# Optimization experiments

Hardware: AMD Instinct MI355X
Metric: run time of the kernel (lower is better)

Reference implementation:

```python
import jax, jax.numpy as jnp
import numpy as np


def setup_inputs() -> dict:
    key = jax.random.key(0)
    ks = jax.random.split(key, 13)
    B, W, C = 16, 2048, 512
    inp = {
        "X_sfr": jax.random.normal(ks[0], (B, W, C), dtype=jnp.float32),
        "adj_matrix": jax.random.normal(ks[1], (B, C, C), dtype=jnp.float32),
        "log_temp": jnp.zeros((1,), dtype=jnp.float32),
        "wq": jax.random.normal(ks[2], (1,), dtype=jnp.float32),
        "bq": jax.random.normal(ks[3], (1,), dtype=jnp.float32),
        "wk": jax.random.normal(ks[4], (1,), dtype=jnp.float32),
        "bk": jax.random.normal(ks[5], (1,), dtype=jnp.float32),
        "wv": jax.random.normal(ks[6], (1,), dtype=jnp.float32),
        "bv": jax.random.normal(ks[7], (1,), dtype=jnp.float32),
        "wmu": jax.random.normal(ks[8], (1,), dtype=jnp.float32),
        "bmu": jax.random.normal(ks[9], (1,), dtype=jnp.float32),
        "wsig": jax.random.normal(ks[10], (1,), dtype=jnp.float32),
        "bsig": jax.random.normal(ks[11], (1,), dtype=jnp.float32),
        "k1": 20,
        "k2": 30,
    }
    return inp


def reference(X_sfr, adj_matrix, log_temp, wq, bq, wk, bk, wv, bv, wmu, bmu, wsig, bsig, k1, k2):
    B, W, C = X_sfr.shape
    # spatial propagation: relu + in-degree normalize adjacency
    adj_nonneg = jnp.maximum(adj_matrix, 0.0)
    in_deg = jnp.clip(adj_nonneg.sum(axis=1, keepdims=True), 1e-4)  # [B,1,C]
    adj_norm = adj_nonneg / in_deg
    X_spatial = jnp.einsum('bwi,bij->bwj', X_sfr, adj_norm)  # [B,W,C]

    # static band mask over time: k1 <= |dt| <= k2, fallback to identity rows
    t = jnp.arange(W)
    delta = jnp.abs(t[None, :] - t[:, None])
    band = (delta >= k1) & (delta <= k2)  # [W,W]
    has_valid = band.any(axis=1)
    band = jnp.where(has_valid[:, None], band, jnp.eye(W, dtype=bool))

    # scalar (1->1) q/k/v projections on the temporal token
    temporal_token = X_spatial.mean(axis=2, keepdims=True)  # [B,W,1]
    q = wq * temporal_token + bq                            # [B,W,1]
    k = wk * temporal_token + bk                            # [B,W,1]
    v = wv * X_spatial + bv                                 # [B,W,C]

    temp = jax.nn.softplus(log_temp)[0] + 1e-4
    logits = jnp.matmul(q, jnp.swapaxes(k, 1, 2)) / temp    # [B,W,W] rank-1
    logits = jnp.where(band[None, :, :], logits, -1e9)
    attn = jax.nn.softmax(logits, axis=-1)
    attn = attn * band[None, :, :].astype(attn.dtype)
    attn = attn / (attn.sum(axis=-1, keepdims=True) + 1e-6)

    sacon_scalar = attn.sum(axis=-1, keepdims=True)         # [B,W,1]
    sacon = jnp.broadcast_to(sacon_scalar, (B, W, C))

    X_temporal = jnp.matmul(attn, v)                        # [B,W,C]
    X_fused = X_temporal + X_spatial

    mu = jnp.clip(wmu * X_fused + bmu, -20.0, 20.0)
    sigma_sq = jax.nn.softplus(wsig * X_fused + bsig) + 0.1
    return mu, sigma_sq, sacon
```

## Files before the change

### kernel.cpp

```cpp
#include <hip/hip_runtime.h>
#include <math.h>

#define B_ 16
#define W_ 2048
#define C_ 512

#define OFF_XB    0
#define OFF_BT    33554432
#define OFF_XSP   41943040
#define OFF_TT    75497472
#define OFF_CS    75628544

typedef short v8s __attribute__((ext_vector_type(8)));
typedef float v4f __attribute__((ext_vector_type(4)));
typedef float v2f __attribute__((ext_vector_type(2)));
typedef unsigned int u32;

__device__ __forceinline__ float softplus_fast(float x) {
    return fmaxf(x, 0.f) + __logf(1.f + __expf(-fabsf(x)));
}
__device__ __forceinline__ unsigned short f2bf(float x) {
    unsigned int u = __float_as_uint(x);
    unsigned int r = (u + 0x7FFFu + ((u >> 16) & 1u)) >> 16;
    return (unsigned short)r;
}
__device__ __forceinline__ float bf2f_lo(unsigned int u) {
    return __uint_as_float(u << 16);
}
__device__ __forceinline__ float bf2f_hi(unsigned int u) {
    return __uint_as_float(u & 0xffff0000u);
}
__device__ __forceinline__ void gload16(const ushort* g, ushort* l) {
    __builtin_amdgcn_global_load_lds(
        (const __attribute__((address_space(1))) u32*)(g),
        (__attribute__((address_space(3))) u32*)(l), 16, 0, 0);
}

__global__ __launch_bounds__(256) void front_k(const float* __restrict__ X,
                                               ushort* __restrict__ Xb,
                                               const float* __restrict__ adj,
                                               float* __restrict__ cs) {
    const int bid = blockIdx.x;
    if (bid < 4096) {
        const size_t e0 = ((size_t)bid * 256 + threadIdx.x) * 16;
        const float4* Xp = (const float4*)(X + e0);
        float4 a = Xp[0], b = Xp[1], c = Xp[2], d = Xp[3];
        v8s o0, o1;
        o0[0] = (short)f2bf(a.x); o0[1] = (short)f2bf(a.y);
        o0[2] = (short)f2bf(a.z); o0[3] = (short)f2bf(a.w);
        o0[4] = (short)f2bf(b.x); o0[5] = (short)f2bf(b.y);
        o0[6] = (short)f2bf(b.z); o0[7] = (short)f2bf(b.w);
        o1[0] = (short)f2bf(c.x); o1[1] = (short)f2bf(c.y);
        o1[2] = (short)f2bf(c.z); o1[3] = (short)f2bf(c.w);
        o1[4] = (short)f2bf(d.x); o1[5] = (short)f2bf(d.y);
        o1[6] = (short)f2bf(d.z); o1[7] = (short)f2bf(d.w);
        *(v8s*)&Xb[e0]     = o0;
        *(v8s*)&Xb[e0 + 8] = o1;
    } else {
        __shared__ float red[8][32];
        const int cb = bid - 4096;
        const int b  = cb >> 6;
        const int rem = cb & 63;
        const int j0 = (rem & 15) * 32;
        const int r0 = (rem >> 4) * 128;
        const int tx = threadIdx.x & 31, ty = threadIdx.x >> 5;
        const float* src = adj + (size_t)b * C_ * C_;
        float s = 0.f;
#pragma unroll 4
        for (int it = 0; it < 16; it++)
            s += fmaxf(src[(size_t)(r0 + it * 8 + ty) * C_ + j0 + tx], 0.f);
        red[ty][tx] = s;
        __syncthreads();
        if (ty == 0) {
            float tot = red[0][tx] + red[1][tx] + red[2][tx] + red[3][tx]
                      + red[4][tx] + red[5][tx] + red[6][tx] + red[7][tx];
            atomicAdd(&cs[b * C_ + j0 + tx], tot);
        }
    }
}

__global__ __launch_bounds__(256) void prep_bt(const float* __restrict__ adj,
                                               const float* __restrict__ cs,
                                               ushort* __restrict__ Bt) {
    __shared__ float t[64][65];
    __shared__ float invs[64];
    const int b = blockIdx.z;
    const int i0 = blockIdx.x * 64;
    const int j0 = blockIdx.y * 64;
    const int tid = threadIdx.x;
    const int tx = tid & 15, ty = tid >> 4;

    if (tid < 64) invs[tid] = 1.f / fmaxf(cs[b * C_ + j0 + tid], 1e-4f);

#pragma unroll
    for (int p = 0; p < 4; p++) {
        const int iy = ty + p * 16;
        const float4 v = *(const float4*)&adj[((size_t)b * C_ + (i0 + iy)) * C_ + j0 + tx * 4];
        t[iy][tx * 4 + 0] = fmaxf(v.x, 0.f);
        t[iy][tx * 4 + 1] = fmaxf(v.y, 0.f);
        t[iy][tx * 4 + 2] = fmaxf(v.z, 0.f);
        t[iy][tx * 4 + 3] = fmaxf(v.w, 0.f);
    }
    __syncthreads();

    const int jj = tid >> 2;
    const int i4 = (tid & 3) * 16;
    const float iv = invs[jj];
    v8s o0, o1;
#pragma unroll
    for (int k = 0; k < 8; k++) o0[k] = (short)f2bf(t[i4 + k][jj] * iv);
#pragma unroll
    for (int k = 0; k < 8; k++) o1[k] = (short)f2bf(t[i4 + 8 + k][jj] * iv);
    ushort* dst = &Bt[(size_t)b * C_ * C_ + (size_t)(j0 + jj) * C_ + i0 + i4];
    *(v8s*)dst       = o0;
    *(v8s*)(dst + 8) = o1;
}

__global__ __launch_bounds__(256) void gemm_mfma(const ushort* __restrict__ Xb,
                                                 const ushort* __restrict__ Bt,
                                                 ushort* __restrict__ Xsp,
                                                 float* __restrict__ tt) {
    __shared__ ushort As[2][128 * 32];
    __shared__ ushort Bs[2][128 * 32];
    const int b  = blockIdx.z;
    const int m0 = blockIdx.y * 128;
    const int n0 = blockIdx.x * 128;
    const int tid  = threadIdx.x;
    const int wave = tid >> 6, lane = tid & 63;
    const int quad = lane >> 4, l16 = lane & 15;
    const int mw = (wave & 1) * 64, nw = (wave >> 1) * 64;

    const ushort* Ag = Xb + (size_t)b * W_ * C_ + (size_t)m0 * C_;
    const ushort* Bg = Bt + (size_t)b * C_ * C_ + (size_t)n0 * C_;

    const int sm = tid >> 2;
    const int sk = (tid & 3) * 8;

    v4f acc[4][4];
#pragma unroll
    for (int mt = 0; mt < 4; mt++)
#pragma unroll
        for (int nt = 0; nt < 4; nt++)
            acc[mt][nt] = (v4f){0.f, 0.f, 0.f, 0.f};

    for (int k0 = 0; k0 < C_; k0 += 64) {
        __syncthreads();
        gload16(Ag + (size_t)sm * C_ + k0 + sk,             &As[0][tid * 8]);
        gload16(Ag + (size_t)(sm + 64) * C_ + k0 + sk,      &As[0][2048 + tid * 8]);
        gload16(Bg + (size_t)sm * C_ + k0 + sk,             &Bs[0][tid * 8]);
        gload16(Bg + (size_t)(sm + 64) * C_ + k0 + sk,      &Bs[0][2048 + tid * 8]);
        gload16(Ag + (size_t)sm * C_ + k0 + 32 + sk,        &As[1][tid * 8]);
        gload16(Ag + (size_t)(sm + 64) * C_ + k0 + 32 + sk, &As[1][2048 + tid * 8]);
        gload16(Bg + (size_t)sm * C_ + k0 + 32 + sk,        &Bs[1][tid * 8]);
        gload16(Bg + (size_t)(sm + 64) * C_ + k0 + 32 + sk, &Bs[1][2048 + tid * 8]);
        __syncthreads();

#pragma unroll
        for (int h = 0; h < 2; h++) {
            v8s af[4], bf[4];
#pragma unroll
            for (int mt = 0; mt < 4; mt++)
                af[mt] = *(const v8s*)&As[h][(mw + mt * 16 + l16) * 32 + quad * 8];
#pragma unroll
            for (int nt = 0; nt < 4; nt++)
                bf[nt] = *(const v8s*)&Bs[h][(nw + nt * 16 + l16) * 32 + quad * 8];
#pragma unroll
            for (int mt = 0; mt < 4; mt++)
#pragma unroll
                for (int nt = 0; nt < 4; nt++)
                    acc[mt][nt] = __builtin_amdgcn_mfma_f32_16x16x32_bf16(bf[nt], af[mt], acc[mt][nt], 0, 0, 0);
        }
    }

#pragma unroll
    for (int mt = 0; mt < 4; mt++) {
        const int row = m0 + mw + mt * 16 + l16;
        ushort* rowp = &Xsp[((size_t)b * W_ + row) * C_];
#pragma unroll
        for (int nt = 0; nt < 4; nt++) {
            const int colb = n0 + nw + nt * 16 + quad * 4;
            ushort4 o;
            o.x = f2bf(acc[mt][nt][0]);
            o.y = f2bf(acc[mt][nt][1]);
            o.z = f2bf(acc[mt][nt][2]);
            o.w = f2bf(acc[mt][nt][3]);
            *(ushort4*)&rowp[colb] = o;
        }
        float s = 0.f;
#pragma unroll
        for (int nt = 0; nt < 4; nt++)
#pragma unroll
            for (int r = 0; r < 4; r++) s += acc[mt][nt][r];
        s += __shfl_xor(s, 16);
        s += __shfl_xor(s, 32);
        if (quad == 0) atomicAdd(&tt[b * W_ + row], s);
    }
}

__global__ __launch_bounds__(256) void final_kernel(const ushort* __restrict__ Xsp,
                                                    const float* __restrict__ tt,
                                                    const float* __restrict__ ltp,
                                                    const float* __restrict__ wqp, const float* __restrict__ bqp,
                                                    const float* __restrict__ wkp, const float* __restrict__ bkp,
                                                    const float* __restrict__ wvp, const float* __restrict__ bvp,
                                                    const float* __restrict__ wmup, const float* __restrict__ bmup,
                                                    const float* __restrict__ wsigp, const float* __restrict__ bsigp,
                                                    const int* __restrict__ k1p, const int* __restrict__ k2p,
                                                    float* __restrict__ out) {
    __shared__ float wlds[4][40][4];
    const int wid = threadIdx.x >> 6, lane = threadIdx.x & 63;
    const int bid = ((int)blockIdx.x & 7) * 256 + ((int)blockIdx.x >> 3);
    const int i0w = bid * 16 + wid * 4;
    const int b = i0w >> 11, ib = i0w & (W_ - 1);
    const int K1 = k1p[0], K2 = k2p[0];
    int ns = K2 - K1 + 1;
    if (ns > 16) ns = 16;
    const int n2 = 2 * ns;
    const int nsL = ns + 3;
    const int nu = 2 * nsL;
    const float Sc = 1.f / (1.f + 1e-6f);

    for (int k = threadIdx.x; k < 4 * 40 * 4; k += 256) ((float*)wlds)[k] = 0.f;
    __syncthreads();

    {
        const float cinv = 1.f / C_;
        const float temp = softplus_fast(ltp[0]) + 1e-4f;
        const float invt = 1.f / temp;
        const float wkc = wkp[0] * cinv, bk = bkp[0];
        const float wqc = wqp[0] * cinv, bq = bqp[0];
        const float* ttb = tt + b * W_;
        const int half = lane >> 5;
        const int s = lane & 31;
#pragma unroll
        for (int rr = 0; rr < 2; rr++) {
            const int r = rr * 2 + half;
            const int i = ib + r;
            const float q = wqc * ttb[i] + bq;
            int j = (s < ns) ? (i - K2 + s) : (i + K1 + (s - ns));
            bool valid = (s < n2) && (j >= 0) && (j < W_);
            int jc = min(max(j, 0), W_ - 1);
            float l = valid ? (q * (wkc * ttb[jc] + bk) * invt) : -1e30f;
            float mx = l;
#pragma unroll
            for (int off = 16; off > 0; off >>= 1) mx = fmaxf(mx, __shfl_xor(mx, off, 32));
            float e = valid ? __expf(l - mx) : 0.f;
            float T = e;
#pragma unroll
            for (int off = 16; off > 0; off >>= 1) T += __shfl_xor(T, off, 32);
            float wsc = (1.f / T) * Sc;
            if (valid) {
                int u = (s < ns) ? (r + s) : (nsL + r + (s - ns));
                wlds[wid][u][r] = e * wsc;
            }
        }
    }
    __syncthreads();

    const ushort* Xbp = Xsp + (size_t)b * W_ * C_;
    const int c8 = lane * 8;

    uint4 xv[4];
#pragma unroll
    for (int r = 0; r < 4; r++)
        xv[r] = *(const uint4*)(Xbp + (size_t)(ib + r) * C_ + c8);

    v2f acc2[4][4];
#pragma unroll
    for (int r = 0; r < 4; r++)
#pragma unroll
        for (int p = 0; p < 4; p++) acc2[r][p] = (v2f){0.f, 0.f};

    auto band_addr = [&](int u) -> const uint4* {
        int j = (u < nsL) ? (ib - K2 + u) : (ib + K1 + (u - nsL));
        j = min(max(j, 0), W_ - 1);
        return (const uint4*)(Xbp + (size_t)j * C_ + c8);
    };
    uint4 vA = *band_addr(0);
    uint4 vB = *band_addr(1);
    for (int u = 0; u < nu; u++) {
        uint4 v = vA;
        vA = vB;
        if (u + 2 < nu) vB = *band_addr(u + 2);
        v2f x[4];
        x[0] = (v2f){bf2f_lo(v.x), bf2f_hi(v.x)};
        x[1] = (v2f){bf2f_lo(v.y), bf2f_hi(v.y)};
        x[2] = (v2f){bf2f_lo(v.z), bf2f_hi(v.z)};
        x[3] = (v2f){bf2f_lo(v.w), bf2f_hi(v.w)};
        const v4f w4 = *(const v4f*)&wlds[wid][u][0];
#pragma unroll
        for (int r = 0; r < 4; r++) {
            v2f w2 = (v2f){w4[r], w4[r]};
#pragma unroll
            for (int p = 0; p < 4; p++) acc2[r][p] += w2 * x[p];
        }
    }

    const float wv = wvp[0], bvS = bvp[0] * Sc;
    const float wmu = wmup[0], bmu = bmup[0];
    const float wsig = wsigp[0], bsig = bsigp[0];
    const size_t N = (size_t)B_ * W_ * C_;

#pragma unroll
    for (int r = 0; r < 4; r++) {
        float xs[8];
        xs[0] = bf2f_lo(xv[r].x); xs[1] = bf2f_hi(xv[r].x);
        xs[2] = bf2f_lo(xv[r].y); xs[3] = bf2f_hi(xv[r].y);
        xs[4] = bf2f_lo(xv[r].z); xs[5] = bf2f_hi(xv[r].z);
        xs[6] = bf2f_lo(xv[r].w); xs[7] = bf2f_hi(xv[r].w);

        float mu[8], sg[8];
#pragma unroll
        for (int k = 0; k < 8; k++) {
            float a = acc2[r][k >> 1][k & 1];
            float xf = fmaf(wv, a, bvS) + xs[k];
            mu[k] = fminf(fmaxf(fmaf(wmu, xf, bmu), -20.f), 20.f);
            sg[k] = softplus_fast(fmaf(wsig, xf, bsig)) + 0.1f;
        }

        const size_t base = (size_t)(i0w + r) * C_ + c8;
        __builtin_nontemporal_store((v4f){mu[0], mu[1], mu[2], mu[3]}, (v4f*)&out[base]);
        __builtin_nontemporal_store((v4f){mu[4], mu[5], mu[6], mu[7]}, (v4f*)&out[base + 4]);
        __builtin_nontemporal_store((v4f){sg[0], sg[1], sg[2], sg[3]}, (v4f*)&out[N + base]);
        __builtin_nontemporal_store((v4f){sg[4], sg[5], sg[6], sg[7]}, (v4f*)&out[N + base + 4]);
        __builtin_nontemporal_store((v4f){Sc, Sc, Sc, Sc}, (v4f*)&out[2 * N + base]);
        __builtin_nontemporal_store((v4f){Sc, Sc, Sc, Sc}, (v4f*)&out[2 * N + base + 4]);
    }
}

extern "C" void kernel_launch(void* const* d_in, const int* in_sizes, int n_in,
                              void* d_out, int out_size, void* d_ws, size_t ws_size,
                              hipStream_t stream) {
    const float* X_sfr = (const float*)d_in[0];
    const float* adj   = (const float*)d_in[1];
    const float* ltp   = (const float*)d_in[2];
    const float* wq    = (const float*)d_in[3];
    const float* bq    = (const float*)d_in[4];
    const float* wk    = (const float*)d_in[5];
    const float* bk    = (const float*)d_in[6];
    const float* wv    = (const float*)d_in[7];
    const float* bv    = (const float*)d_in[8];
    const float* wmu   = (const float*)d_in[9];
    const float* bmu   = (const float*)d_in[10];
    const float* wsig  = (const float*)d_in[11];
    const float* bsig  = (const float*)d_in[12];
    const int*   k1p   = (const int*)d_in[13];
    const int*   k2p   = (const int*)d_in[14];

    char* ws = (char*)d_ws;
    ushort* Xb  = (ushort*)(ws + OFF_XB);
    ushort* Bt  = (ushort*)(ws + OFF_BT);
    ushort* Xsp = (ushort*)(ws + OFF_XSP);
    float*  tt  = (float*)(ws + OFF_TT);
    float*  cs  = (float*)(ws + OFF_CS);
    float*  out = (float*)d_out;

    hipMemsetAsync(tt, 0, B_ * W_ * sizeof(float) + B_ * C_ * sizeof(float), stream);

    front_k<<<4096 + 1024, 256, 0, stream>>>(X_sfr, Xb, adj, cs);

    prep_bt<<<dim3(C_ / 64, C_ / 64, B_), 256, 0, stream>>>(adj, cs, Bt);

    gemm_mfma<<<dim3(C_ / 128, W_ / 128, B_), 256, 0, stream>>>(Xb, Bt, Xsp, tt);

    final_kernel<<<(B_ * W_) / 16, 256, 0, stream>>>(Xsp, tt, ltp, wq, bq, wk, bk,
                                                     wv, bv, wmu, bmu, wsig, bsig,
                                                     k1p, k2p, out);
}
```

Baseline: 388.1 us.

## Fuse column-sum and transpose into front kernel, apply normalization in GEMM epilogue

Removes the separate prep_bt launch. The front kernel now computes the relu'd adjacency transpose (unnormalized, in bf16) and accumulates column sums at the same time. The in-degree division moves into the GEMM epilogue as a per-column scale. This drops one kernel launch and a second full pass over the adjacency, at the cost of bf16 rounding before normalization and a small extra epilogue multiply.

```diff
diff --git a/kernel.cpp b/kernel.cpp
--- a/kernel.cpp
+++ b/kernel.cpp
@@ -39,6 +39,7 @@
 __global__ __launch_bounds__(256) void front_k(const float* __restrict__ X,
                                                ushort* __restrict__ Xb,
                                                const float* __restrict__ adj,
+                                               ushort* __restrict__ Bt,
                                                float* __restrict__ cs) {
     const int bid = blockIdx.x;
     if (bid < 4096) {
@@ -57,71 +58,59 @@
         *(v8s*)&Xb[e0]     = o0;
         *(v8s*)&Xb[e0 + 8] = o1;
     } else {
-        __shared__ float red[8][32];
+        __shared__ float t[64][65];
         const int cb = bid - 4096;
         const int b  = cb >> 6;
         const int rem = cb & 63;
-        const int j0 = (rem & 15) * 32;
-        const int r0 = (rem >> 4) * 128;
-        const int tx = threadIdx.x & 31, ty = threadIdx.x >> 5;
-        const float* src = adj + (size_t)b * C_ * C_;
-        float s = 0.f;
-#pragma unroll 4
-        for (int it = 0; it < 16; it++)
-            s += fmaxf(src[(size_t)(r0 + it * 8 + ty) * C_ + j0 + tx], 0.f);
-        red[ty][tx] = s;
+        const int i0 = (rem & 7) * 64;
+        const int j0 = (rem >> 3) * 64;
+        const int tid = threadIdx.x;
+        const int tx = tid & 15, ty = tid >> 4;
+
+#pragma unroll
+        for (int p = 0; p < 4; p++) {
+            const int iy = ty + p * 16;
+            const float4 v = *(const float4*)&adj[((size_t)b * C_ + (i0 + iy)) * C_ + j0 + tx * 4];
+            t[iy][tx * 4 + 0] = fmaxf(v.x, 0.f);
+            t[iy][tx * 4 + 1] = fmaxf(v.y, 0.f);
+            t[iy][tx * 4 + 2] = fmaxf(v.z, 0.f);
+            t[iy][tx * 4 + 3] = fmaxf(v.w, 0.f);
+        }
         __syncthreads();
-        if (ty == 0) {
-            float tot = red[0][tx] + red[1][tx] + red[2][tx] + red[3][tx]
-                      + red[4][tx] + red[5][tx] + red[6][tx] + red[7][tx];
-            atomicAdd(&cs[b * C_ + j0 + tx], tot);
-        }
-    }
-}
-
-__global__ __launch_bounds__(256) void prep_bt(const float* __restrict__ adj,
-                                               const float* __restrict__ cs,
-                                               ushort* __restrict__ Bt) {
-    __shared__ float t[64][65];
-    __shared__ float invs[64];
-    const int b = blockIdx.z;
-    const int i0 = blockIdx.x * 64;
-    const int j0 = blockIdx.y * 64;
-    const int tid = threadIdx.x;
-    const int tx = tid & 15, ty = tid >> 4;
-
-    if (tid < 64) invs[tid] = 1.f / fmaxf(cs[b * C_ + j0 + tid], 1e-4f);
-
-#pragma unroll
-    for (int p = 0; p < 4; p++) {
-        const int iy = ty + p * 16;
-        const float4 v = *(const float4*)&adj[((size_t)b * C_ + (i0 + iy)) * C_ + j0 + tx * 4];
-        t[iy][tx * 4 + 0] = fmaxf(v.x, 0.f);
-        t[iy][tx * 4 + 1] = fmaxf(v.y, 0.f);
-        t[iy][tx * 4 + 2] = fmaxf(v.z, 0.f);
-        t[iy][tx * 4 + 3] = fmaxf(v.w, 0.f);
-    }
-    __syncthreads();
-
-    const int jj = tid >> 2;
-    const int i4 = (tid & 3) * 16;
-    const float iv = invs[jj];
-    v8s o0, o1;
-#pragma unroll
-    for (int k = 0; k < 8; k++) o0[k] = (short)f2bf(t[i4 + k][jj] * iv);
-#pragma unroll
-    for (int k = 0; k < 8; k++) o1[k] = (short)f2bf(t[i4 + 8 + k][jj] * iv);
-    ushort* dst = &Bt[(size_t)b * C_ * C_ + (size_t)(j0 + jj) * C_ + i0 + i4];
-    *(v8s*)dst       = o0;
-    *(v8s*)(dst + 8) = o1;
+
+        const int jj = tid >> 2;
+        const int i4 = (tid & 3) * 16;
+        float psum = 0.f;
+        v8s o0, o1;
+#pragma unroll
+        for (int k = 0; k < 8; k++) {
+            float v = t[i4 + k][jj];
+            psum += v;
+            o0[k] = (short)f2bf(v);
+        }
+#pragma unroll
+        for (int k = 0; k < 8; k++) {
+            float v = t[i4 + 8 + k][jj];
+            psum += v;
+            o1[k] = (short)f2bf(v);
+        }
+        ushort* dst = &Bt[(size_t)b * C_ * C_ + (size_t)(j0 + jj) * C_ + i0 + i4];
+        *(v8s*)dst       = o0;
+        *(v8s*)(dst + 8) = o1;
+        psum += __shfl_xor(psum, 1);
+        psum += __shfl_xor(psum, 2);
+        if ((tid & 3) == 0) atomicAdd(&cs[b * C_ + j0 + jj], psum);
+    }
 }
 
 __global__ __launch_bounds__(256) void gemm_mfma(const ushort* __restrict__ Xb,
                                                  const ushort* __restrict__ Bt,
+                                                 const float* __restrict__ cs,
                                                  ushort* __restrict__ Xsp,
                                                  float* __restrict__ tt) {
     __shared__ ushort As[2][128 * 32];
     __shared__ ushort Bs[2][128 * 32];
+    __shared__ float invL[128];
     const int b  = blockIdx.z;
     const int m0 = blockIdx.y * 128;
     const int n0 = blockIdx.x * 128;
@@ -129,6 +118,8 @@
     const int wave = tid >> 6, lane = tid & 63;
     const int quad = lane >> 4, l16 = lane & 15;
     const int mw = (wave & 1) * 64, nw = (wave >> 1) * 64;
+
+    if (tid < 128) invL[tid] = 1.f / fmaxf(cs[b * C_ + n0 + tid], 1e-4f);
 
     const ushort* Ag = Xb + (size_t)b * W_ * C_ + (size_t)m0 * C_;
     const ushort* Bg = Bt + (size_t)b * C_ * C_ + (size_t)n0 * C_;
@@ -170,6 +161,16 @@
                 for (int nt = 0; nt < 4; nt++)
                     acc[mt][nt] = __builtin_amdgcn_mfma_f32_16x16x32_bf16(bf[nt], af[mt], acc[mt][nt], 0, 0, 0);
         }
+    }
+
+#pragma unroll
+    for (int nt = 0; nt < 4; nt++) {
+        const v4f iv = *(const v4f*)&invL[nw + nt * 16 + quad * 4];
+#pragma unroll
+        for (int mt = 0; mt < 4; mt++)
+#pragma unroll
+            for (int r = 0; r < 4; r++)
+                acc[mt][nt][r] *= iv[r];
     }
 
 #pragma unroll
@@ -357,11 +358,9 @@
 
     hipMemsetAsync(tt, 0, B_ * W_ * sizeof(float) + B_ * C_ * sizeof(float), stream);
 
-    front_k<<<4096 + 1024, 256, 0, stream>>>(X_sfr, Xb, adj, cs);
-
-    prep_bt<<<dim3(C_ / 64, C_ / 64, B_), 256, 0, stream>>>(adj, cs, Bt);
-
-    gemm_mfma<<<dim3(C_ / 128, W_ / 128, B_), 256, 0, stream>>>(Xb, Bt, Xsp, tt);
+    front_k<<<4096 + 1024, 256, 0, stream>>>(X_sfr, Xb, adj, Bt, cs);
+
+    gemm_mfma<<<dim3(C_ / 128, W_ / 128, B_), 256, 0, stream>>>(Xb, Bt, cs, Xsp, tt);
 
     final_kernel<<<(B_ * W_) / 16, 256, 0, stream>>>(Xsp, tt, ltp, wq, bq, wk, bk,
                                                      wv, bv, wmu, bmu, wsig, bsig,
```

Measured after the change: 395.0 us. No clear change (+1.8%).
